# Optimization experiments

Measured on AMD Instinct MI355X. Metric: run time of the kernel, lower is better.

Reference implementation:

```python
import jax, jax.numpy as jnp
import numpy as np

N_FFT = 512
HOP = 256
FS = 16000
D_INTER = 0.04
C_SOUND = 343.0
SOURCE_NUM = 2
EST_NUM = 4      # TF snapshots for the spatial covariance
T_START = 120    # starting frame of the snapshots
EPS = 1e-8
N_ANGLES = 361   # theta in [-90, 90] deg
T_SAMPLES = 3200000
N_MICS = 4


def _stft(xc):
    """xc: (C, T) real -> X: (C, F, n_frames) complex64.
    Matches torch.stft(center=True, pad_mode='reflect', onesided=True)
    with window = hann(N_FFT, periodic=True) ** 0.5.
    """
    n = jnp.arange(N_FFT, dtype=xc.dtype)
    win = jnp.sqrt(0.5 * (1.0 - jnp.cos(2.0 * jnp.pi * n / N_FFT)))  # hann^0.5
    pad = N_FFT // 2
    xp = jnp.pad(xc, ((0, 0), (pad, pad)), mode='reflect')
    n_frames = 1 + xc.shape[1] // HOP
    idx = jnp.arange(n_frames)[:, None] * HOP + jnp.arange(N_FFT)[None, :]
    frames = xp[:, idx] * win                     # (C, n_frames, N_FFT)
    X = jnp.fft.rfft(frames, axis=-1)             # (C, n_frames, F)
    return jnp.swapaxes(X, 1, 2)                  # (C, F, n_frames)


def setup_inputs() -> dict:
    key = jax.random.key(0)
    x = jax.random.normal(key, (T_SAMPLES, N_MICS), dtype=jnp.float32)
    return {"x": x}


def reference(x) -> jnp.ndarray:
    # ---- multi-channel STFT ----
    X = _stft(x.T)                                # (M, F, T_frames) complex64
    M = X.shape[0]

    # ---- spatial covariance from EST_NUM snapshots (vectorized over bins) ----
    Xs = X[:, :, T_START:T_START + EST_NUM]       # (M, F, EST_NUM)
    spt = jnp.einsum('mft,nft->fmn', Xs, jnp.conj(Xs)) / EST_NUM  # (F, M, M) Hermitian

    # ---- noise subspace via Hermitian eigendecomposition ----
    # eigh returns ascending eigenvalues; take the M-SOURCE_NUM smallest
    # (noise) eigenvectors, i.e. descending order then columns SOURCE_NUM:.
    _, V = jnp.linalg.eigh(spt)                   # (F, M, M)
    noise = V[:, :, ::-1][:, :, SOURCE_NUM:]      # (F, M, M-SOURCE_NUM)

    # ---- spatial spectrum, fully batched over all 361 angles ----
    f_analog = jnp.linspace(0.0, FS / 2, N_FFT // 2 + 1, dtype=jnp.float32)
    theta = jnp.deg2rad(jnp.linspace(-90.0, 90.0, N_ANGLES, dtype=jnp.float32))
    mics = jnp.arange(M, dtype=jnp.float32)
    # phase: (A, F, M)
    phase = (2.0 * jnp.pi * D_INTER / C_SOUND) * (
        jnp.sin(theta)[:, None, None] * f_analog[None, :, None] * mics[None, None, :]
    )
    steer = jnp.exp(-1j * phase).astype(jnp.complex64)            # (A, F, M)
    mid = jnp.einsum('afm,fmk->afk', steer, noise)                # (A, F, K)
    val = jnp.sum(mid.real ** 2 + mid.imag ** 2, axis=-1)         # (A, F)
    spt_spec = jnp.mean(1.0 / (val + EPS), axis=1)                # (A,)
    return spt_spec
```

## Files before the change

kernel.cpp:

```cpp
#include <hip/hip_runtime.h>
#include <math.h>

#define NFFT   512
#define HOP    256
#define NFREQ  257
#define NMIC   4
#define TSTART 120
#define NANG   361

static constexpr double PI_D = 3.14159265358979323846;
static constexpr float  PI_F = 3.14159265358979323846f;

__global__ __launch_bounds__(512)
void stft_kernel(const float* __restrict__ x,
                 float* __restrict__ part_re,
                 float* __restrict__ part_im) {
    int b = blockIdx.x;
    int chunk = b >> 4;
    int m = (b >> 2) & 3;
    int t = b & 3;
    int tid = threadIdx.x;

    __shared__ float2 tw[512];
    __shared__ float  v[128];

    {
        float ang = (2.0f * PI_F / 512.0f) * (float)tid;
        float s, c;
        sincosf(ang, &s, &c);
        tw[tid] = make_float2(c, s);
    }
    if (tid < 128) {
        int n = chunk * 128 + tid;
        long base = ((long)(TSTART + t - 1) * HOP) * NMIC + m;
        v[tid] = x[base + (long)n * NMIC] * sinf(PI_F * (float)n / 512.0f);
    }
    __syncthreads();

    int f = tid;
    if (f >= NFREQ) return;
    int k = (f * (chunk * 128)) & 511;
    float re = 0.0f, im = 0.0f;
#pragma unroll 4
    for (int j = 0; j < 128; ++j) {
        float vn = v[j];
        float2 cs = tw[k];
        re += vn * cs.x;
        im -= vn * cs.y;
        k = (k + f) & 511;
    }
    int id = f * 16 + m * 4 + t;
    part_re[chunk * 4112 + id] = re;
    part_im[chunk * 4112 + id] = im;
}

__global__ __launch_bounds__(64)
void eig_kernel(const float* __restrict__ part_re,
                const float* __restrict__ part_im,
                float* __restrict__ coef) {
    int f = blockIdx.x * blockDim.x + threadIdx.x;
    if (f >= NFREQ) return;

    float Xr[4][4], Xi[4][4];
#pragma unroll
    for (int m = 0; m < 4; ++m)
#pragma unroll
        for (int t = 0; t < 4; ++t) {
            int id = f * 16 + m * 4 + t;
            Xr[m][t] = part_re[id] + part_re[4112 + id]
                     + part_re[2 * 4112 + id] + part_re[3 * 4112 + id];
            Xi[m][t] = part_im[id] + part_im[4112 + id]
                     + part_im[2 * 4112 + id] + part_im[3 * 4112 + id];
        }

    float Ar[4][4], Ai[4][4];
#pragma unroll
    for (int m = 0; m < 4; ++m)
#pragma unroll
        for (int n = 0; n < 4; ++n) {
            float rr = 0.0f, ii = 0.0f;
#pragma unroll
            for (int t = 0; t < 4; ++t) {
                rr += Xr[m][t] * Xr[n][t] + Xi[m][t] * Xi[n][t];
                ii += Xi[m][t] * Xr[n][t] - Xr[m][t] * Xi[n][t];
            }
            Ar[m][n] = rr;
            Ai[m][n] = ii;
        }

    float Vr[4][4] = {{1,0,0,0},{0,1,0,0},{0,0,1,0},{0,0,0,1}};
    float Vi[4][4] = {{0,0,0,0},{0,0,0,0},{0,0,0,0},{0,0,0,0}};

    for (int sweep = 0; sweep < 6; ++sweep) {
#pragma unroll
        for (int p = 0; p < 3; ++p)
#pragma unroll
            for (int q = p + 1; q < 4; ++q) {
                float ar = Ar[p][q], ai = Ai[p][q];
                float n2 = ar * ar + ai * ai;
                bool ok = n2 > 1e-24f;
                float n2s = ok ? n2 : 1.0f;
                float inv = 1.0f / sqrtf(n2s);
                float er = ar * inv, ei = ai * inv;
                float tau = (Ar[q][q] - Ar[p][p]) * (0.5f * inv * (ok ? 1.0f : 0.0f));
                float t_ = (tau >= 0.0f ? 1.0f : -1.0f) /
                           (fabsf(tau) + sqrtf(1.0f + tau * tau));
                float c = ok ? 1.0f / sqrtf(1.0f + t_ * t_) : 1.0f;
                float s = ok ? t_ * c : 0.0f;
#pragma unroll
                for (int k = 0; k < 4; ++k) {
                    float apr = Ar[k][p], api = Ai[k][p];
                    float aqr = Ar[k][q], aqi = Ai[k][q];
                    float tr = er * aqr + ei * aqi;
                    float ti = er * aqi - ei * aqr;
                    Ar[k][p] = c * apr - s * tr;
                    Ai[k][p] = c * api - s * ti;
                    float ur = er * apr - ei * api;
                    float ui = er * api + ei * apr;
                    Ar[k][q] = s * ur + c * aqr;
                    Ai[k][q] = s * ui + c * aqi;
                }
#pragma unroll
                for (int k = 0; k < 4; ++k) {
                    float apr = Ar[p][k], api = Ai[p][k];
                    float aqr = Ar[q][k], aqi = Ai[q][k];
                    float tr = er * aqr - ei * aqi;
                    float ti = er * aqi + ei * aqr;
                    Ar[p][k] = c * apr - s * tr;
                    Ai[p][k] = c * api - s * ti;
                    float ur = er * apr + ei * api;
                    float ui = er * api - ei * apr;
                    Ar[q][k] = s * ur + c * aqr;
                    Ai[q][k] = s * ui + c * aqi;
                }
#pragma unroll
                for (int k = 0; k < 4; ++k) {
                    float apr = Vr[k][p], api = Vi[k][p];
                    float aqr = Vr[k][q], aqi = Vi[k][q];
                    float tr = er * aqr + ei * aqi;
                    float ti = er * aqi - ei * aqr;
                    Vr[k][p] = c * apr - s * tr;
                    Vi[k][p] = c * api - s * ti;
                    float ur = er * apr - ei * api;
                    float ui = er * api + ei * apr;
                    Vr[k][q] = s * ur + c * aqr;
                    Vi[k][q] = s * ui + c * aqi;
                }
            }
    }

    float dd[4] = {Ar[0][0], Ar[1][1], Ar[2][2], Ar[3][3]};
    float w[4];
#pragma unroll
    for (int j = 0; j < 4; ++j) {
        int rank = 0;
#pragma unroll
        for (int k = 0; k < 4; ++k) {
            if (k == j) continue;
            bool less = (dd[k] < dd[j]) || (dd[k] == dd[j] && k < j);
            rank += less ? 1 : 0;
        }
        w[j] = (rank < 2) ? 1.0f : 0.0f;
    }

    float s1r = 0.f, s1i = 0.f, s2r = 0.f, s2i = 0.f, s3r = 0.f, s3i = 0.f, trc = 0.f;
#pragma unroll
    for (int j = 0; j < 4; ++j) {
        float wj = w[j];
        s1r += wj * (Vr[0][j]*Vr[1][j] + Vi[0][j]*Vi[1][j]
                   + Vr[1][j]*Vr[2][j] + Vi[1][j]*Vi[2][j]
                   + Vr[2][j]*Vr[3][j] + Vi[2][j]*Vi[3][j]);
        s1i += wj * (Vi[0][j]*Vr[1][j] - Vr[0][j]*Vi[1][j]
                   + Vi[1][j]*Vr[2][j] - Vr[1][j]*Vi[2][j]
                   + Vi[2][j]*Vr[3][j] - Vr[2][j]*Vi[3][j]);
        s2r += wj * (Vr[0][j]*Vr[2][j] + Vi[0][j]*Vi[2][j]
                   + Vr[1][j]*Vr[3][j] + Vi[1][j]*Vi[3][j]);
        s2i += wj * (Vi[0][j]*Vr[2][j] - Vr[0][j]*Vi[2][j]
                   + Vi[1][j]*Vr[3][j] - Vr[1][j]*Vi[3][j]);
        s3r += wj * (Vr[0][j]*Vr[3][j] + Vi[0][j]*Vi[3][j]);
        s3i += wj * (Vi[0][j]*Vr[3][j] - Vr[0][j]*Vi[3][j]);
        trc += wj * (Vr[0][j]*Vr[0][j] + Vi[0][j]*Vi[0][j]
                   + Vr[1][j]*Vr[1][j] + Vi[1][j]*Vi[1][j]
                   + Vr[2][j]*Vr[2][j] + Vi[2][j]*Vi[2][j]
                   + Vr[3][j]*Vr[3][j] + Vi[3][j]*Vi[3][j]);
    }
    float* cf = coef + f * 8;
    cf[0] = s1r; cf[1] = s1i; cf[2] = s2r; cf[3] = s2i;
    cf[4] = s3r; cf[5] = s3i; cf[6] = trc; cf[7] = 0.0f;
}

__global__ __launch_bounds__(320)
void music_kernel(const float* __restrict__ coef,
                  float* __restrict__ out) {
    int a = blockIdx.x;
    int tid = threadIdx.x;
    float r = 0.0f;
    if (tid < NFREQ) {
        const float4* cf4 = (const float4*)(coef + tid * 8);
        float4 cA = cf4[0];
        float4 cB = cf4[1];
        float theta = (-90.0f + 0.5f * (float)a) * (PI_F / 180.0f);
        float freq = 31.25f * (float)tid;
        float phi = (float)(2.0 * PI_D * 0.04 / 343.0) * sinf(theta) * freq;
        float s1, c1;
        sincosf(phi, &s1, &c1);
        float c2 = c1 * c1 - s1 * s1;
        float s2 = 2.0f * s1 * c1;
        float c3 = c1 * c2 - s1 * s2;
        float s3 = s1 * c2 + c1 * s2;
        float val = cB.z + 2.0f * (c1 * cA.x - s1 * cA.y
                                 + c2 * cA.z - s2 * cA.w
                                 + c3 * cB.x - s3 * cB.y);
        r = 1.0f / (val + 1e-8f);
    }
#pragma unroll
    for (int off = 32; off > 0; off >>= 1)
        r += __shfl_down(r, off, 64);
    __shared__ float ps[5];
    if ((tid & 63) == 0) ps[tid >> 6] = r;
    __syncthreads();
    if (tid == 0)
        out[a] = (ps[0] + ps[1] + ps[2] + ps[3] + ps[4]) / 257.0f;
}

extern "C" void kernel_launch(void* const* d_in, const int* in_sizes, int n_in,
                              void* d_out, int out_size, void* d_ws, size_t ws_size,
                              hipStream_t stream) {
    const float* x = (const float*)d_in[0];
    float* out = (float*)d_out;

    float* part_re = (float*)d_ws;
    float* part_im = part_re + 4 * 4112;
    float* coef    = part_im + 4 * 4112;

    stft_kernel<<<64, 512, 0, stream>>>(x, part_re, part_im);
    eig_kernel<<<(NFREQ + 63) / 64, 64, 0, stream>>>(part_re, part_im, coef);
    music_kernel<<<NANG, 320, 0, stream>>>(coef, out);
}
```

Measured before the change: 108.5 us.

## Fuse eigendecomposition into MUSIC spectrum kernel, recomputing per angle block

Merges the per-frequency Jacobi eigendecomposition kernel into the angle-spectrum kernel, so each of the 361 angle blocks recomputes the noise-subspace coefficients for all 257 bins in registers. This removes one kernel launch and the global round trip for the coefficient buffer. In exchange, the eigen-solve is done redundantly 361 times. It also runs at 512 threads per block under higher register pressure, which can lengthen per-block latency.

After: 170.9 us. 1.58x slower.

```diff
diff --git a/kernel.cpp b/kernel.cpp
--- a/kernel.cpp
+++ b/kernel.cpp
@@ -54,153 +54,143 @@
     part_im[chunk * 4112 + id] = im;
 }
 
-__global__ __launch_bounds__(64)
-void eig_kernel(const float* __restrict__ part_re,
-                const float* __restrict__ part_im,
-                float* __restrict__ coef) {
-    int f = blockIdx.x * blockDim.x + threadIdx.x;
-    if (f >= NFREQ) return;
-
-    float Xr[4][4], Xi[4][4];
-#pragma unroll
-    for (int m = 0; m < 4; ++m)
-#pragma unroll
-        for (int t = 0; t < 4; ++t) {
-            int id = f * 16 + m * 4 + t;
-            Xr[m][t] = part_re[id] + part_re[4112 + id]
-                     + part_re[2 * 4112 + id] + part_re[3 * 4112 + id];
-            Xi[m][t] = part_im[id] + part_im[4112 + id]
-                     + part_im[2 * 4112 + id] + part_im[3 * 4112 + id];
-        }
-
-    float Ar[4][4], Ai[4][4];
-#pragma unroll
-    for (int m = 0; m < 4; ++m)
-#pragma unroll
-        for (int n = 0; n < 4; ++n) {
-            float rr = 0.0f, ii = 0.0f;
-#pragma unroll
-            for (int t = 0; t < 4; ++t) {
-                rr += Xr[m][t] * Xr[n][t] + Xi[m][t] * Xi[n][t];
-                ii += Xi[m][t] * Xr[n][t] - Xr[m][t] * Xi[n][t];
-            }
-            Ar[m][n] = rr;
-            Ai[m][n] = ii;
-        }
-
-    float Vr[4][4] = {{1,0,0,0},{0,1,0,0},{0,0,1,0},{0,0,0,1}};
-    float Vi[4][4] = {{0,0,0,0},{0,0,0,0},{0,0,0,0},{0,0,0,0}};
-
-    for (int sweep = 0; sweep < 6; ++sweep) {
-#pragma unroll
-        for (int p = 0; p < 3; ++p)
-#pragma unroll
-            for (int q = p + 1; q < 4; ++q) {
-                float ar = Ar[p][q], ai = Ai[p][q];
-                float n2 = ar * ar + ai * ai;
-                bool ok = n2 > 1e-24f;
-                float n2s = ok ? n2 : 1.0f;
-                float inv = 1.0f / sqrtf(n2s);
-                float er = ar * inv, ei = ai * inv;
-                float tau = (Ar[q][q] - Ar[p][p]) * (0.5f * inv * (ok ? 1.0f : 0.0f));
-                float t_ = (tau >= 0.0f ? 1.0f : -1.0f) /
-                           (fabsf(tau) + sqrtf(1.0f + tau * tau));
-                float c = ok ? 1.0f / sqrtf(1.0f + t_ * t_) : 1.0f;
-                float s = ok ? t_ * c : 0.0f;
-#pragma unroll
-                for (int k = 0; k < 4; ++k) {
-                    float apr = Ar[k][p], api = Ai[k][p];
-                    float aqr = Ar[k][q], aqi = Ai[k][q];
-                    float tr = er * aqr + ei * aqi;
-                    float ti = er * aqi - ei * aqr;
-                    Ar[k][p] = c * apr - s * tr;
-                    Ai[k][p] = c * api - s * ti;
-                    float ur = er * apr - ei * api;
-                    float ui = er * api + ei * apr;
-                    Ar[k][q] = s * ur + c * aqr;
-                    Ai[k][q] = s * ui + c * aqi;
-                }
-#pragma unroll
-                for (int k = 0; k < 4; ++k) {
-                    float apr = Ar[p][k], api = Ai[p][k];
-                    float aqr = Ar[q][k], aqi = Ai[q][k];
-                    float tr = er * aqr - ei * aqi;
-                    float ti = er * aqi + ei * aqr;
-                    Ar[p][k] = c * apr - s * tr;
-                    Ai[p][k] = c * api - s * ti;
-                    float ur = er * apr + ei * api;
-                    float ui = er * api - ei * apr;
-                    Ar[q][k] = s * ur + c * aqr;
-                    Ai[q][k] = s * ui + c * aqi;
-                }
-#pragma unroll
-                for (int k = 0; k < 4; ++k) {
-                    float apr = Vr[k][p], api = Vi[k][p];
-                    float aqr = Vr[k][q], aqi = Vi[k][q];
-                    float tr = er * aqr + ei * aqi;
-                    float ti = er * aqi - ei * aqr;
-                    Vr[k][p] = c * apr - s * tr;
-                    Vi[k][p] = c * api - s * ti;
-                    float ur = er * apr - ei * api;
-                    float ui = er * api + ei * apr;
-                    Vr[k][q] = s * ur + c * aqr;
-                    Vi[k][q] = s * ui + c * aqi;
-                }
-            }
-    }
-
-    float dd[4] = {Ar[0][0], Ar[1][1], Ar[2][2], Ar[3][3]};
-    float w[4];
-#pragma unroll
-    for (int j = 0; j < 4; ++j) {
-        int rank = 0;
-#pragma unroll
-        for (int k = 0; k < 4; ++k) {
-            if (k == j) continue;
-            bool less = (dd[k] < dd[j]) || (dd[k] == dd[j] && k < j);
-            rank += less ? 1 : 0;
-        }
-        w[j] = (rank < 2) ? 1.0f : 0.0f;
-    }
-
-    float s1r = 0.f, s1i = 0.f, s2r = 0.f, s2i = 0.f, s3r = 0.f, s3i = 0.f, trc = 0.f;
-#pragma unroll
-    for (int j = 0; j < 4; ++j) {
-        float wj = w[j];
-        s1r += wj * (Vr[0][j]*Vr[1][j] + Vi[0][j]*Vi[1][j]
-                   + Vr[1][j]*Vr[2][j] + Vi[1][j]*Vi[2][j]
-                   + Vr[2][j]*Vr[3][j] + Vi[2][j]*Vi[3][j]);
-        s1i += wj * (Vi[0][j]*Vr[1][j] - Vr[0][j]*Vi[1][j]
-                   + Vi[1][j]*Vr[2][j] - Vr[1][j]*Vi[2][j]
-                   + Vi[2][j]*Vr[3][j] - Vr[2][j]*Vi[3][j]);
-        s2r += wj * (Vr[0][j]*Vr[2][j] + Vi[0][j]*Vi[2][j]
-                   + Vr[1][j]*Vr[3][j] + Vi[1][j]*Vi[3][j]);
-        s2i += wj * (Vi[0][j]*Vr[2][j] - Vr[0][j]*Vi[2][j]
-                   + Vi[1][j]*Vr[3][j] - Vr[1][j]*Vi[3][j]);
-        s3r += wj * (Vr[0][j]*Vr[3][j] + Vi[0][j]*Vi[3][j]);
-        s3i += wj * (Vi[0][j]*Vr[3][j] - Vr[0][j]*Vi[3][j]);
-        trc += wj * (Vr[0][j]*Vr[0][j] + Vi[0][j]*Vi[0][j]
-                   + Vr[1][j]*Vr[1][j] + Vi[1][j]*Vi[1][j]
-                   + Vr[2][j]*Vr[2][j] + Vi[2][j]*Vi[2][j]
-                   + Vr[3][j]*Vr[3][j] + Vi[3][j]*Vi[3][j]);
-    }
-    float* cf = coef + f * 8;
-    cf[0] = s1r; cf[1] = s1i; cf[2] = s2r; cf[3] = s2i;
-    cf[4] = s3r; cf[5] = s3i; cf[6] = trc; cf[7] = 0.0f;
-}
-
-__global__ __launch_bounds__(320)
-void music_kernel(const float* __restrict__ coef,
-                  float* __restrict__ out) {
+__global__ __launch_bounds__(512)
+void eig_music_kernel(const float* __restrict__ part_re,
+                      const float* __restrict__ part_im,
+                      float* __restrict__ out) {
     int a = blockIdx.x;
     int tid = threadIdx.x;
+
     float r = 0.0f;
     if (tid < NFREQ) {
-        const float4* cf4 = (const float4*)(coef + tid * 8);
-        float4 cA = cf4[0];
-        float4 cB = cf4[1];
+        int f = tid;
+
+        float Xr[4][4], Xi[4][4];
+#pragma unroll
+        for (int m = 0; m < 4; ++m)
+#pragma unroll
+            for (int t = 0; t < 4; ++t) {
+                int id = f * 16 + m * 4 + t;
+                Xr[m][t] = part_re[id] + part_re[4112 + id]
+                         + part_re[2 * 4112 + id] + part_re[3 * 4112 + id];
+                Xi[m][t] = part_im[id] + part_im[4112 + id]
+                         + part_im[2 * 4112 + id] + part_im[3 * 4112 + id];
+            }
+
+        float Ar[4][4], Ai[4][4];
+#pragma unroll
+        for (int m = 0; m < 4; ++m)
+#pragma unroll
+            for (int n = 0; n < 4; ++n) {
+                float rr = 0.0f, ii = 0.0f;
+#pragma unroll
+                for (int t = 0; t < 4; ++t) {
+                    rr += Xr[m][t] * Xr[n][t] + Xi[m][t] * Xi[n][t];
+                    ii += Xi[m][t] * Xr[n][t] - Xr[m][t] * Xi[n][t];
+                }
+                Ar[m][n] = rr;
+                Ai[m][n] = ii;
+            }
+
+        float Vr[4][4] = {{1,0,0,0},{0,1,0,0},{0,0,1,0},{0,0,0,1}};
+        float Vi[4][4] = {{0,0,0,0},{0,0,0,0},{0,0,0,0},{0,0,0,0}};
+
+        for (int sweep = 0; sweep < 6; ++sweep) {
+#pragma unroll
+            for (int p = 0; p < 3; ++p)
+#pragma unroll
+                for (int q = p + 1; q < 4; ++q) {
+                    float ar = Ar[p][q], ai = Ai[p][q];
+                    float n2 = ar * ar + ai * ai;
+                    bool ok = n2 > 1e-24f;
+                    float n2s = ok ? n2 : 1.0f;
+                    float inv = 1.0f / sqrtf(n2s);
+                    float er = ar * inv, ei = ai * inv;
+                    float tau = (Ar[q][q] - Ar[p][p]) * (0.5f * inv * (ok ? 1.0f : 0.0f));
+                    float t_ = (tau >= 0.0f ? 1.0f : -1.0f) /
+                               (fabsf(tau) + sqrtf(1.0f + tau * tau));
+                    float c = ok ? 1.0f / sqrtf(1.0f + t_ * t_) : 1.0f;
+                    float s = ok ? t_ * c : 0.0f;
+#pragma unroll
+                    for (int k = 0; k < 4; ++k) {
+                        float apr = Ar[k][p], api = Ai[k][p];
+                        float aqr = Ar[k][q], aqi = Ai[k][q];
+                        float tr = er * aqr + ei * aqi;
+                        float ti = er * aqi - ei * aqr;
+                        Ar[k][p] = c * apr - s * tr;
+                        Ai[k][p] = c * api - s * ti;
+                        float ur = er * apr - ei * api;
+                        float ui = er * api + ei * apr;
+                        Ar[k][q] = s * ur + c * aqr;
+                        Ai[k][q] = s * ui + c * aqi;
+                    }
+#pragma unroll
+                    for (int k = 0; k < 4; ++k) {
+                        float apr = Ar[p][k], api = Ai[p][k];
+                        float aqr = Ar[q][k], aqi = Ai[q][k];
+                        float tr = er * aqr - ei * aqi;
+                        float ti = er * aqi + ei * aqr;
+                        Ar[p][k] = c * apr - s * tr;
+                        Ai[p][k] = c * api - s * ti;
+                        float ur = er * apr + ei * api;
+                        float ui = er * api - ei * apr;
+                        Ar[q][k] = s * ur + c * aqr;
+                        Ai[q][k] = s * ui + c * aqi;
+                    }
+#pragma unroll
+                    for (int k = 0; k < 4; ++k) {
+                        float apr = Vr[k][p], api = Vi[k][p];
+                        float aqr = Vr[k][q], aqi = Vi[k][q];
+                        float tr = er * aqr + ei * aqi;
+                        float ti = er * aqi - ei * aqr;
+                        Vr[k][p] = c * apr - s * tr;
+                        Vi[k][p] = c * api - s * ti;
+                        float ur = er * apr - ei * api;
+                        float ui = er * api + ei * apr;
+                        Vr[k][q] = s * ur + c * aqr;
+                        Vi[k][q] = s * ui + c * aqi;
+                    }
+                }
+        }
+
+        float dd[4] = {Ar[0][0], Ar[1][1], Ar[2][2], Ar[3][3]};
+        float w[4];
+#pragma unroll
+        for (int j = 0; j < 4; ++j) {
+            int rank = 0;
+#pragma unroll
+            for (int k = 0; k < 4; ++k) {
+                if (k == j) continue;
+                bool less = (dd[k] < dd[j]) || (dd[k] == dd[j] && k < j);
+                rank += less ? 1 : 0;
+            }
+            w[j] = (rank < 2) ? 1.0f : 0.0f;
+        }
+
+        float s1r = 0.f, s1i = 0.f, s2r = 0.f, s2i = 0.f, s3r = 0.f, s3i = 0.f, trc = 0.f;
+#pragma unroll
+        for (int j = 0; j < 4; ++j) {
+            float wj = w[j];
+            s1r += wj * (Vr[0][j]*Vr[1][j] + Vi[0][j]*Vi[1][j]
+                       + Vr[1][j]*Vr[2][j] + Vi[1][j]*Vi[2][j]
+                       + Vr[2][j]*Vr[3][j] + Vi[2][j]*Vi[3][j]);
+            s1i += wj * (Vi[0][j]*Vr[1][j] - Vr[0][j]*Vi[1][j]
+                       + Vi[1][j]*Vr[2][j] - Vr[1][j]*Vi[2][j]
+                       + Vi[2][j]*Vr[3][j] - Vr[2][j]*Vi[3][j]);
+            s2r += wj * (Vr[0][j]*Vr[2][j] + Vi[0][j]*Vi[2][j]
+                       + Vr[1][j]*Vr[3][j] + Vi[1][j]*Vi[3][j]);
+            s2i += wj * (Vi[0][j]*Vr[2][j] - Vr[0][j]*Vi[2][j]
+                       + Vi[1][j]*Vr[3][j] - Vr[1][j]*Vi[3][j]);
+            s3r += wj * (Vr[0][j]*Vr[3][j] + Vi[0][j]*Vi[3][j]);
+            s3i += wj * (Vi[0][j]*Vr[3][j] - Vr[0][j]*Vi[3][j]);
+            trc += wj * (Vr[0][j]*Vr[0][j] + Vi[0][j]*Vi[0][j]
+                       + Vr[1][j]*Vr[1][j] + Vi[1][j]*Vi[1][j]
+                       + Vr[2][j]*Vr[2][j] + Vi[2][j]*Vi[2][j]
+                       + Vr[3][j]*Vr[3][j] + Vi[3][j]*Vi[3][j]);
+        }
+
         float theta = (-90.0f + 0.5f * (float)a) * (PI_F / 180.0f);
-        float freq = 31.25f * (float)tid;
+        float freq = 31.25f * (float)f;
         float phi = (float)(2.0 * PI_D * 0.04 / 343.0) * sinf(theta) * freq;
         float s1, c1;
         sincosf(phi, &s1, &c1);
@@ -208,19 +198,21 @@
         float s2 = 2.0f * s1 * c1;
         float c3 = c1 * c2 - s1 * s2;
         float s3 = s1 * c2 + c1 * s2;
-        float val = cB.z + 2.0f * (c1 * cA.x - s1 * cA.y
-                                 + c2 * cA.z - s2 * cA.w
-                                 + c3 * cB.x - s3 * cB.y);
+        float val = trc + 2.0f * (c1 * s1r - s1 * s1i
+                                + c2 * s2r - s2 * s2i
+                                + c3 * s3r - s3 * s3i);
         r = 1.0f / (val + 1e-8f);
     }
+
 #pragma unroll
     for (int off = 32; off > 0; off >>= 1)
         r += __shfl_down(r, off, 64);
-    __shared__ float ps[5];
+    __shared__ float ps[8];
     if ((tid & 63) == 0) ps[tid >> 6] = r;
     __syncthreads();
     if (tid == 0)
-        out[a] = (ps[0] + ps[1] + ps[2] + ps[3] + ps[4]) / 257.0f;
+        out[a] = (ps[0] + ps[1] + ps[2] + ps[3]
+                + ps[4] + ps[5] + ps[6] + ps[7]) / 257.0f;
 }
 
 extern "C" void kernel_launch(void* const* d_in, const int* in_sizes, int n_in,
@@ -231,9 +223,7 @@
 
     float* part_re = (float*)d_ws;
     float* part_im = part_re + 4 * 4112;
-    float* coef    = part_im + 4 * 4112;
 
     stft_kernel<<<64, 512, 0, stream>>>(x, part_re, part_im);
-    eig_kernel<<<(NFREQ + 63) / 64, 64, 0, stream>>>(part_re, part_im, coef);
-    music_kernel<<<NANG, 320, 0, stream>>>(coef, out);
+    eig_music_kernel<<<NANG, 512, 0, stream>>>(part_re, part_im, out);
 }
```

## Fuse STFT and eigendecomposition into one kernel over frequency groups

Applied to the files above, without the earlier changes.

Merges the STFT partial-DFT kernel and the per-bin Jacobi eigen kernel into one launch of 17 blocks, each covering 16 frequency bins. Each block stages the needed input samples for all mics and snapshots in shared memory and computes full 512-point DFT sums per (mic, frame, bin), then runs the eigensolver on 16 threads. This removes one kernel launch and the global round-trip of the partial sums, at the cost of far fewer blocks, longer serial loops per thread, and redundant window and twiddle setup in every block.

Result: slower. 130.4 us (+20.2%).

```diff
diff --git a/kernel.cpp b/kernel.cpp
--- a/kernel.cpp
+++ b/kernel.cpp
@@ -7,186 +7,184 @@
 #define NMIC   4
 #define TSTART 120
 #define NANG   361
+#define FG     16
+#define NBLK   17
 
 static constexpr double PI_D = 3.14159265358979323846;
 static constexpr float  PI_F = 3.14159265358979323846f;
 
-__global__ __launch_bounds__(512)
-void stft_kernel(const float* __restrict__ x,
-                 float* __restrict__ part_re,
-                 float* __restrict__ part_im) {
-    int b = blockIdx.x;
-    int chunk = b >> 4;
-    int m = (b >> 2) & 3;
-    int t = b & 3;
+__global__ __launch_bounds__(256, 1)
+void stft_eig_kernel(const float* __restrict__ x,
+                     float* __restrict__ coef) {
     int tid = threadIdx.x;
-
+    int fl  = tid & 15;
+    int mt  = tid >> 4;
+    int m   = mt >> 2;
+    int t   = mt & 3;
+    int f   = blockIdx.x * FG + fl;
+
+    __shared__ float  xl[1280 * 4];
+    __shared__ float  win[512];
     __shared__ float2 tw[512];
-    __shared__ float  v[128];
+    __shared__ float  Xre[16][16];
+    __shared__ float  Xim[16][16];
 
     {
-        float ang = (2.0f * PI_F / 512.0f) * (float)tid;
+        const float4* xv = (const float4*)(x + 30464 * 4);
+        float4* xl4 = (float4*)xl;
+        for (int i = tid; i < 1280; i += 256) xl4[i] = xv[i];
+    }
+    for (int i = tid; i < 512; i += 256) {
+        win[i] = sinf(PI_F * (float)i / 512.0f);
         float s, c;
-        sincosf(ang, &s, &c);
-        tw[tid] = make_float2(c, s);
-    }
-    if (tid < 128) {
-        int n = chunk * 128 + tid;
-        long base = ((long)(TSTART + t - 1) * HOP) * NMIC + m;
-        v[tid] = x[base + (long)n * NMIC] * sinf(PI_F * (float)n / 512.0f);
+        sincosf((2.0f * PI_F / 512.0f) * (float)i, &s, &c);
+        tw[i] = make_float2(c, s);
     }
     __syncthreads();
 
-    int f = tid;
-    if (f >= NFREQ) return;
-    int k = (f * (chunk * 128)) & 511;
     float re = 0.0f, im = 0.0f;
-#pragma unroll 4
-    for (int j = 0; j < 128; ++j) {
-        float vn = v[j];
-        float2 cs = tw[k];
-        re += vn * cs.x;
-        im -= vn * cs.y;
-        k = (k + f) & 511;
-    }
-    int id = f * 16 + m * 4 + t;
-    part_re[chunk * 4112 + id] = re;
-    part_im[chunk * 4112 + id] = im;
-}
-
-__global__ __launch_bounds__(64)
-void eig_kernel(const float* __restrict__ part_re,
-                const float* __restrict__ part_im,
-                float* __restrict__ coef) {
-    int f = blockIdx.x * blockDim.x + threadIdx.x;
-    if (f >= NFREQ) return;
-
-    float Xr[4][4], Xi[4][4];
-#pragma unroll
-    for (int m = 0; m < 4; ++m)
-#pragma unroll
-        for (int t = 0; t < 4; ++t) {
-            int id = f * 16 + m * 4 + t;
-            Xr[m][t] = part_re[id] + part_re[4112 + id]
-                     + part_re[2 * 4112 + id] + part_re[3 * 4112 + id];
-            Xi[m][t] = part_im[id] + part_im[4112 + id]
-                     + part_im[2 * 4112 + id] + part_im[3 * 4112 + id];
-        }
-
-    float Ar[4][4], Ai[4][4];
-#pragma unroll
-    for (int m = 0; m < 4; ++m)
-#pragma unroll
-        for (int n = 0; n < 4; ++n) {
-            float rr = 0.0f, ii = 0.0f;
-#pragma unroll
-            for (int t = 0; t < 4; ++t) {
-                rr += Xr[m][t] * Xr[n][t] + Xi[m][t] * Xi[n][t];
-                ii += Xi[m][t] * Xr[n][t] - Xr[m][t] * Xi[n][t];
+    if (f < NFREQ) {
+        int toff = t * 256;
+        int k = 0;
+#pragma unroll 8
+        for (int n = 0; n < 512; ++n) {
+            float v = xl[(toff + n) * 4 + m] * win[n];
+            float2 cs = tw[k];
+            re += v * cs.x;
+            im -= v * cs.y;
+            k = (k + f) & 511;
+        }
+    }
+    Xre[mt][fl] = re;
+    Xim[mt][fl] = im;
+    __syncthreads();
+
+    int ff = blockIdx.x * FG + tid;
+    if (tid < 16 && ff < NFREQ) {
+        float Xr[4][4], Xi[4][4];
+#pragma unroll
+        for (int mm = 0; mm < 4; ++mm)
+#pragma unroll
+            for (int tt = 0; tt < 4; ++tt) {
+                Xr[mm][tt] = Xre[mm * 4 + tt][tid];
+                Xi[mm][tt] = Xim[mm * 4 + tt][tid];
             }
-            Ar[m][n] = rr;
-            Ai[m][n] = ii;
-        }
-
-    float Vr[4][4] = {{1,0,0,0},{0,1,0,0},{0,0,1,0},{0,0,0,1}};
-    float Vi[4][4] = {{0,0,0,0},{0,0,0,0},{0,0,0,0},{0,0,0,0}};
-
-    for (int sweep = 0; sweep < 6; ++sweep) {
-#pragma unroll
-        for (int p = 0; p < 3; ++p)
-#pragma unroll
-            for (int q = p + 1; q < 4; ++q) {
-                float ar = Ar[p][q], ai = Ai[p][q];
-                float n2 = ar * ar + ai * ai;
-                bool ok = n2 > 1e-24f;
-                float n2s = ok ? n2 : 1.0f;
-                float inv = 1.0f / sqrtf(n2s);
-                float er = ar * inv, ei = ai * inv;
-                float tau = (Ar[q][q] - Ar[p][p]) * (0.5f * inv * (ok ? 1.0f : 0.0f));
-                float t_ = (tau >= 0.0f ? 1.0f : -1.0f) /
-                           (fabsf(tau) + sqrtf(1.0f + tau * tau));
-                float c = ok ? 1.0f / sqrtf(1.0f + t_ * t_) : 1.0f;
-                float s = ok ? t_ * c : 0.0f;
-#pragma unroll
-                for (int k = 0; k < 4; ++k) {
-                    float apr = Ar[k][p], api = Ai[k][p];
-                    float aqr = Ar[k][q], aqi = Ai[k][q];
-                    float tr = er * aqr + ei * aqi;
-                    float ti = er * aqi - ei * aqr;
-                    Ar[k][p] = c * apr - s * tr;
-                    Ai[k][p] = c * api - s * ti;
-                    float ur = er * apr - ei * api;
-                    float ui = er * api + ei * apr;
-                    Ar[k][q] = s * ur + c * aqr;
-                    Ai[k][q] = s * ui + c * aqi;
+
+        float Ar[4][4], Ai[4][4];
+#pragma unroll
+        for (int mm = 0; mm < 4; ++mm)
+#pragma unroll
+            for (int nn = 0; nn < 4; ++nn) {
+                float rr = 0.0f, ii = 0.0f;
+#pragma unroll
+                for (int tt = 0; tt < 4; ++tt) {
+                    rr += Xr[mm][tt] * Xr[nn][tt] + Xi[mm][tt] * Xi[nn][tt];
+                    ii += Xi[mm][tt] * Xr[nn][tt] - Xr[mm][tt] * Xi[nn][tt];
                 }
-#pragma unroll
-                for (int k = 0; k < 4; ++k) {
-                    float apr = Ar[p][k], api = Ai[p][k];
-                    float aqr = Ar[q][k], aqi = Ai[q][k];
-                    float tr = er * aqr - ei * aqi;
-                    float ti = er * aqi + ei * aqr;
-                    Ar[p][k] = c * apr - s * tr;
-                    Ai[p][k] = c * api - s * ti;
-                    float ur = er * apr + ei * api;
-                    float ui = er * api - ei * apr;
-                    Ar[q][k] = s * ur + c * aqr;
-                    Ai[q][k] = s * ui + c * aqi;
+                Ar[mm][nn] = rr;
+                Ai[mm][nn] = ii;
+            }
+
+        float Vr[4][4] = {{1,0,0,0},{0,1,0,0},{0,0,1,0},{0,0,0,1}};
+        float Vi[4][4] = {{0,0,0,0},{0,0,0,0},{0,0,0,0},{0,0,0,0}};
+
+        for (int sweep = 0; sweep < 6; ++sweep) {
+#pragma unroll
+            for (int p = 0; p < 3; ++p)
+#pragma unroll
+                for (int q = p + 1; q < 4; ++q) {
+                    float ar = Ar[p][q], ai = Ai[p][q];
+                    float n2 = ar * ar + ai * ai;
+                    bool ok = n2 > 1e-24f;
+                    float n2s = ok ? n2 : 1.0f;
+                    float inv = 1.0f / sqrtf(n2s);
+                    float er = ar * inv, ei = ai * inv;
+                    float tau = (Ar[q][q] - Ar[p][p]) * (0.5f * inv * (ok ? 1.0f : 0.0f));
+                    float t_ = (tau >= 0.0f ? 1.0f : -1.0f) /
+                               (fabsf(tau) + sqrtf(1.0f + tau * tau));
+                    float c = ok ? 1.0f / sqrtf(1.0f + t_ * t_) : 1.0f;
+                    float s = ok ? t_ * c : 0.0f;
+#pragma unroll
+                    for (int k = 0; k < 4; ++k) {
+                        float apr = Ar[k][p], api = Ai[k][p];
+                        float aqr = Ar[k][q], aqi = Ai[k][q];
+                        float tr = er * aqr + ei * aqi;
+                        float ti = er * aqi - ei * aqr;
+                        Ar[k][p] = c * apr - s * tr;
+                        Ai[k][p] = c * api - s * ti;
+                        float ur = er * apr - ei * api;
+                        float ui = er * api + ei * apr;
+                        Ar[k][q] = s * ur + c * aqr;
+                        Ai[k][q] = s * ui + c * aqi;
+                    }
+#pragma unroll
+                    for (int k = 0; k < 4; ++k) {
+                        float apr = Ar[p][k], api = Ai[p][k];
+                        float aqr = Ar[q][k], aqi = Ai[q][k];
+                        float tr = er * aqr - ei * aqi;
+                        float ti = er * aqi + ei * aqr;
+                        Ar[p][k] = c * apr - s * tr;
+                        Ai[p][k] = c * api - s * ti;
+                        float ur = er * apr + ei * api;
+                        float ui = er * api - ei * apr;
+                        Ar[q][k] = s * ur + c * aqr;
+                        Ai[q][k] = s * ui + c * aqi;
+                    }
+#pragma unroll
+                    for (int k = 0; k < 4; ++k) {
+                        float apr = Vr[k][p], api = Vi[k][p];
+                        float aqr = Vr[k][q], aqi = Vi[k][q];
+                        float tr = er * aqr + ei * aqi;
+                        float ti = er * aqi - ei * aqr;
+                        Vr[k][p] = c * apr - s * tr;
+                        Vi[k][p] = c * api - s * ti;
+                        float ur = er * apr - ei * api;
+                        float ui = er * api + ei * apr;
+                        Vr[k][q] = s * ur + c * aqr;
+                        Vi[k][q] = s * ui + c * aqi;
+                    }
                 }
-#pragma unroll
-                for (int k = 0; k < 4; ++k) {
-                    float apr = Vr[k][p], api = Vi[k][p];
-                    float aqr = Vr[k][q], aqi = Vi[k][q];
-                    float tr = er * aqr + ei * aqi;
-                    float ti = er * aqi - ei * aqr;
-                    Vr[k][p] = c * apr - s * tr;
-                    Vi[k][p] = c * api - s * ti;
-                    float ur = er * apr - ei * api;
-                    float ui = er * api + ei * apr;
-                    Vr[k][q] = s * ur + c * aqr;
-                    Vi[k][q] = s * ui + c * aqi;
-                }
+        }
+
+        float dd[4] = {Ar[0][0], Ar[1][1], Ar[2][2], Ar[3][3]};
+        float w[4];
+#pragma unroll
+        for (int j = 0; j < 4; ++j) {
+            int rank = 0;
+#pragma unroll
+            for (int k = 0; k < 4; ++k) {
+                if (k == j) continue;
+                bool less = (dd[k] < dd[j]) || (dd[k] == dd[j] && k < j);
+                rank += less ? 1 : 0;
             }
-    }
-
-    float dd[4] = {Ar[0][0], Ar[1][1], Ar[2][2], Ar[3][3]};
-    float w[4];
-#pragma unroll
-    for (int j = 0; j < 4; ++j) {
-        int rank = 0;
-#pragma unroll
-        for (int k = 0; k < 4; ++k) {
-            if (k == j) continue;
-            bool less = (dd[k] < dd[j]) || (dd[k] == dd[j] && k < j);
-            rank += less ? 1 : 0;
-        }
-        w[j] = (rank < 2) ? 1.0f : 0.0f;
-    }
-
-    float s1r = 0.f, s1i = 0.f, s2r = 0.f, s2i = 0.f, s3r = 0.f, s3i = 0.f, trc = 0.f;
-#pragma unroll
-    for (int j = 0; j < 4; ++j) {
-        float wj = w[j];
-        s1r += wj * (Vr[0][j]*Vr[1][j] + Vi[0][j]*Vi[1][j]
-                   + Vr[1][j]*Vr[2][j] + Vi[1][j]*Vi[2][j]
-                   + Vr[2][j]*Vr[3][j] + Vi[2][j]*Vi[3][j]);
-        s1i += wj * (Vi[0][j]*Vr[1][j] - Vr[0][j]*Vi[1][j]
-                   + Vi[1][j]*Vr[2][j] - Vr[1][j]*Vi[2][j]
-                   + Vi[2][j]*Vr[3][j] - Vr[2][j]*Vi[3][j]);
-        s2r += wj * (Vr[0][j]*Vr[2][j] + Vi[0][j]*Vi[2][j]
-                   + Vr[1][j]*Vr[3][j] + Vi[1][j]*Vi[3][j]);
-        s2i += wj * (Vi[0][j]*Vr[2][j] - Vr[0][j]*Vi[2][j]
-                   + Vi[1][j]*Vr[3][j] - Vr[1][j]*Vi[3][j]);
-        s3r += wj * (Vr[0][j]*Vr[3][j] + Vi[0][j]*Vi[3][j]);
-        s3i += wj * (Vi[0][j]*Vr[3][j] - Vr[0][j]*Vi[3][j]);
-        trc += wj * (Vr[0][j]*Vr[0][j] + Vi[0][j]*Vi[0][j]
-                   + Vr[1][j]*Vr[1][j] + Vi[1][j]*Vi[1][j]
-                   + Vr[2][j]*Vr[2][j] + Vi[2][j]*Vi[2][j]
-                   + Vr[3][j]*Vr[3][j] + Vi[3][j]*Vi[3][j]);
-    }
-    float* cf = coef + f * 8;
-    cf[0] = s1r; cf[1] = s1i; cf[2] = s2r; cf[3] = s2i;
-    cf[4] = s3r; cf[5] = s3i; cf[6] = trc; cf[7] = 0.0f;
+            w[j] = (rank < 2) ? 1.0f : 0.0f;
+        }
+
+        float s1r = 0.f, s1i = 0.f, s2r = 0.f, s2i = 0.f, s3r = 0.f, s3i = 0.f, trc = 0.f;
+#pragma unroll
+        for (int j = 0; j < 4; ++j) {
+            float wj = w[j];
+            s1r += wj * (Vr[0][j]*Vr[1][j] + Vi[0][j]*Vi[1][j]
+                       + Vr[1][j]*Vr[2][j] + Vi[1][j]*Vi[2][j]
+                       + Vr[2][j]*Vr[3][j] + Vi[2][j]*Vi[3][j]);
+            s1i += wj * (Vi[0][j]*Vr[1][j] - Vr[0][j]*Vi[1][j]
+                       + Vi[1][j]*Vr[2][j] - Vr[1][j]*Vi[2][j]
+                       + Vi[2][j]*Vr[3][j] - Vr[2][j]*Vi[3][j]);
+            s2r += wj * (Vr[0][j]*Vr[2][j] + Vi[0][j]*Vi[2][j]
+                       + Vr[1][j]*Vr[3][j] + Vi[1][j]*Vi[3][j]);
+            s2i += wj * (Vi[0][j]*Vr[2][j] - Vr[0][j]*Vi[2][j]
+                       + Vi[1][j]*Vr[3][j] - Vr[1][j]*Vi[3][j]);
+            s3r += wj * (Vr[0][j]*Vr[3][j] + Vi[0][j]*Vi[3][j]);
+            s3i += wj * (Vi[0][j]*Vr[3][j] - Vr[0][j]*Vi[3][j]);
+            trc += wj * (Vr[0][j]*Vr[0][j] + Vi[0][j]*Vi[0][j]
+                       + Vr[1][j]*Vr[1][j] + Vi[1][j]*Vi[1][j]
+                       + Vr[2][j]*Vr[2][j] + Vi[2][j]*Vi[2][j]
+                       + Vr[3][j]*Vr[3][j] + Vi[3][j]*Vi[3][j]);
+        }
+        float* cf = coef + ff * 8;
+        cf[0] = s1r; cf[1] = s1i; cf[2] = s2r; cf[3] = s2i;
+        cf[4] = s3r; cf[5] = s3i; cf[6] = trc; cf[7] = 0.0f;
+    }
 }
 
 __global__ __launch_bounds__(320)
@@ -228,12 +226,8 @@
                               hipStream_t stream) {
     const float* x = (const float*)d_in[0];
     float* out = (float*)d_out;
-
-    float* part_re = (float*)d_ws;
-    float* part_im = part_re + 4 * 4112;
-    float* coef    = part_im + 4 * 4112;
-
-    stft_kernel<<<64, 512, 0, stream>>>(x, part_re, part_im);
-    eig_kernel<<<(NFREQ + 63) / 64, 64, 0, stream>>>(part_re, part_im, coef);
+    float* coef = (float*)d_ws;
+
+    stft_eig_kernel<<<NBLK, 256, 0, stream>>>(x, coef);
     music_kernel<<<NANG, 320, 0, stream>>>(coef, out);
 }
```
